# Kernel tuning notes

Measured on AMD Instinct MI355X. Metric: run time of the kernel, lower is better.

The kernel has to match this reference:

```python
import jax, jax.numpy as jnp
import numpy as np

HEADS = 8
EPS = 1e-5


def setup_inputs() -> dict:
    key = jax.random.key(0)
    ks = jax.random.split(key, 8)
    B, S, D = 4, 2048, 512
    inputs = jax.random.normal(ks[0], (B, S, D), dtype=jnp.float32)
    mask = jnp.ones((B, S), dtype=jnp.int32)
    sc = 1.0 / np.sqrt(D)
    # torch Linear weights stored transposed as [in, out] for x @ W
    W_qkv = jax.random.uniform(ks[1], (D, 3 * D), jnp.float32, -sc, sc)
    b_qkv = jax.random.uniform(ks[2], (3 * D,), jnp.float32, -sc, sc)
    W_o = jax.random.uniform(ks[3], (D, D), jnp.float32, -sc, sc)
    b_o = jax.random.uniform(ks[4], (D,), jnp.float32, -sc, sc)
    gamma = jnp.ones((D,), jnp.float32)
    beta = jnp.zeros((D,), jnp.float32)
    return {"inputs": inputs, "mask": mask, "W_qkv": W_qkv, "b_qkv": b_qkv,
            "W_o": W_o, "b_o": b_o, "gamma": gamma, "beta": beta}


def reference(inputs, mask, W_qkv, b_qkv, W_o, b_o, gamma, beta):
    B, S, D = inputs.shape
    H = HEADS
    dh = D // H
    t = inputs @ W_qkv + b_qkv                      # [B,S,3D]
    q, k, v = jnp.split(t, 3, axis=-1)
    # [B,S,D] -> [B,H,S,dh]
    q = q.reshape(B, S, H, dh).transpose(0, 2, 1, 3)
    k = k.reshape(B, S, H, dh).transpose(0, 2, 1, 3)
    v = v.reshape(B, S, H, dh).transpose(0, 2, 1, 3)
    # unscaled dot-product attention (is_scaled=False in the source)
    scores = jnp.einsum('bhqd,bhkd->bhqk', q, k)    # [B,H,S,S]
    key_mask = (mask > 0)[:, None, None, :]         # broadcast over heads & query rows
    scores = jnp.where(key_mask, scores, -jnp.inf)
    attn = jax.nn.softmax(scores, axis=-1)
    att = jnp.einsum('bhqk,bhkd->bhqd', attn, v)    # [B,H,S,dh]
    att = att.transpose(0, 2, 1, 3).reshape(B, S, D)
    out = att @ W_o + b_o
    x = out + att                                    # residual
    mu = jnp.mean(x, axis=-1, keepdims=True)
    var = jnp.mean(jnp.square(x - mu), axis=-1, keepdims=True)
    return (x - mu) / jnp.sqrt(var + EPS) * gamma + beta
```

## Files before the change

kernel.cpp:

```cpp
#include <hip/hip_runtime.h>
#include <cstdint>

#define S_LEN 2048
#define D_MODEL 512
#define H_NUM 8
#define DH 64
#define LOG2E 1.4426950408889634f

typedef __attribute__((ext_vector_type(8))) short bf16x8;
typedef __attribute__((ext_vector_type(8))) unsigned short u16x8;
typedef __attribute__((ext_vector_type(4))) float f32x4;

__device__ inline unsigned short f2bf(float x) {
    unsigned int u = __builtin_bit_cast(unsigned int, x);
    u += 0x7fffu + ((u >> 16) & 1u);
    return (unsigned short)(u >> 16);
}
__device__ inline float bf2f(unsigned short u) {
    return __builtin_bit_cast(float, (unsigned int)u << 16);
}
__device__ inline unsigned pack_bf2(float a, float b) {
    unsigned ua = __builtin_bit_cast(unsigned, a) + 0x8000u;
    unsigned ub = __builtin_bit_cast(unsigned, b) + 0x8000u;
    return __builtin_amdgcn_perm(ub, ua, 0x07060302);
}

__device__ inline void async_ld16(const unsigned short* g, unsigned short* l) {
    __builtin_amdgcn_global_load_lds(
        (const __attribute__((address_space(1))) unsigned int*)(const unsigned int*)g,
        (__attribute__((address_space(3))) unsigned int*)(unsigned int*)l,
        16, 0, 0);
}

__global__ __launch_bounds__(256) void prep(
    const float* __restrict__ X, const float* __restrict__ Wqkv,
    const float* __restrict__ Wo,
    unsigned short* __restrict__ Xb, unsigned short* __restrict__ WqkvT,
    unsigned short* __restrict__ WoT)
{
    __shared__ float tile[32][36];
    const int blk = blockIdx.x;
    const int tid = threadIdx.x;
    if (blk < 1024) {
        const int base = blk * 4096 + tid * 16;
        #pragma unroll
        for (int i = 0; i < 4; ++i) {
            float4 v = *(const float4*)(X + base + i * 4);
            ushort4 o;
            o.x = f2bf(v.x); o.y = f2bf(v.y); o.z = f2bf(v.z); o.w = f2bf(v.w);
            *(ushort4*)(Xb + base + i * 4) = o;
        }
        return;
    }
    const float* src; unsigned short* dst; int N, t;
    if (blk < 1792) { src = Wqkv; dst = WqkvT; N = 1536; t = blk - 1024; }
    else            { src = Wo;   dst = WoT;   N = 512;  t = blk - 1792; }
    const int tnx = N / 32;
    const int bx = t % tnx;
    const int by = t / tnx;
    const int row = tid >> 3;
    const int c4  = (tid & 7) * 4;
    *(float4*)&tile[row][c4] = *(const float4*)(src + (size_t)(by * 32 + row) * N + bx * 32 + c4);
    __syncthreads();
    ushort4 o;
    o.x = f2bf(tile[c4 + 0][row]);
    o.y = f2bf(tile[c4 + 1][row]);
    o.z = f2bf(tile[c4 + 2][row]);
    o.w = f2bf(tile[c4 + 3][row]);
    *(ushort4*)(dst + (size_t)(bx * 32 + row) * 512 + by * 32 + c4) = o;
}

__global__ __launch_bounds__(256) void qkv_mfma(
    const unsigned short* __restrict__ Xb, const unsigned short* __restrict__ WT,
    const float* __restrict__ bias,
    unsigned short* __restrict__ Q, unsigned short* __restrict__ K,
    unsigned short* __restrict__ Vt)
{
    __shared__ unsigned short sA[128 * 64];
    __shared__ unsigned short sB[128 * 64];
    const int tid  = threadIdx.x;
    const int w    = tid >> 6;
    const int lane = tid & 63;
    const int l16  = lane & 15;
    const int quad = lane >> 4;
    const int wm = w >> 1, wn = w & 1;
    const int n0 = blockIdx.x * 128;
    const int m0 = blockIdx.y * 128;

    const unsigned short* gA[4]; const unsigned short* gB[4];
    unsigned short *lA[4], *lB[4];
    #pragma unroll
    for (int j = 0; j < 4; ++j) {
        const int ci = tid + j * 256;
        const int row = ci >> 3;
        const int col = ((ci & 7) ^ (row & 7)) * 8;
        gA[j] = Xb + (size_t)(m0 + row) * 512 + col;
        gB[j] = WT + (size_t)(n0 + row) * 512 + col;
        lA[j] = sA + ci * 8 - lane * 8;
        lB[j] = sB + ci * 8 - lane * 8;
    }

    f32x4 acc[4][4] = {};
    for (int k0 = 0; k0 < 512; k0 += 64) {
        __syncthreads();
        #pragma unroll
        for (int j = 0; j < 4; ++j) {
            async_ld16(gA[j] + k0, lA[j]);
            async_ld16(gB[j] + k0, lB[j]);
        }
        __syncthreads();
        bf16x8 a[4][2], bfr[4][2];
        #pragma unroll
        for (int mi = 0; mi < 4; ++mi) {
            const int row = wm * 64 + mi * 16 + l16;
            a[mi][0] = *(const bf16x8*)&sA[row * 64 + ((quad       ^ (row & 7)) * 8)];
            a[mi][1] = *(const bf16x8*)&sA[row * 64 + (((4 + quad) ^ (row & 7)) * 8)];
        }
        #pragma unroll
        for (int ni = 0; ni < 4; ++ni) {
            const int row = wn * 64 + ni * 16 + l16;
            bfr[ni][0] = *(const bf16x8*)&sB[row * 64 + ((quad       ^ (row & 7)) * 8)];
            bfr[ni][1] = *(const bf16x8*)&sB[row * 64 + (((4 + quad) ^ (row & 7)) * 8)];
        }
        #pragma unroll
        for (int mi = 0; mi < 4; ++mi)
            #pragma unroll
            for (int ni = 0; ni < 4; ++ni) {
                acc[mi][ni] = __builtin_amdgcn_mfma_f32_16x16x32_bf16(a[mi][0], bfr[ni][0], acc[mi][ni], 0, 0, 0);
                acc[mi][ni] = __builtin_amdgcn_mfma_f32_16x16x32_bf16(a[mi][1], bfr[ni][1], acc[mi][ni], 0, 0, 0);
            }
    }

    const int which = n0 >> 9;
    const int h = ((n0 & 511) >> 6) + wn;
    const int b = m0 >> 11;
    const int sbase = (m0 & 2047) + wm * 64;
    float bv[4];
    #pragma unroll
    for (int ni = 0; ni < 4; ++ni) bv[ni] = bias[n0 + wn * 64 + ni * 16 + l16];
    if (which == 2) {
        #pragma unroll
        for (int ni = 0; ni < 4; ++ni) {
            const int dh = ni * 16 + l16;
            unsigned short* vp = Vt + ((size_t)(b * H_NUM + h) * DH + dh) * S_LEN;
            #pragma unroll
            for (int mi = 0; mi < 4; ++mi) {
                const int s0 = sbase + mi * 16 + quad * 4;
                ushort4 o;
                o.x = f2bf(acc[mi][ni][0] + bv[ni]);
                o.y = f2bf(acc[mi][ni][1] + bv[ni]);
                o.z = f2bf(acc[mi][ni][2] + bv[ni]);
                o.w = f2bf(acc[mi][ni][3] + bv[ni]);
                *(ushort4*)(vp + s0) = o;
            }
        }
    } else {
        const float qs = (which == 0) ? LOG2E : 1.0f;
        unsigned short* dst = (which == 0) ? Q : K;
        dst += (size_t)(b * H_NUM + h) * S_LEN * DH;
        #pragma unroll
        for (int mi = 0; mi < 4; ++mi)
            #pragma unroll
            for (int r = 0; r < 4; ++r) {
                const int s = sbase + mi * 16 + quad * 4 + r;
                #pragma unroll
                for (int ni = 0; ni < 4; ++ni)
                    dst[(size_t)s * DH + ni * 16 + l16] = f2bf((acc[mi][ni][r] + bv[ni]) * qs);
            }
    }
}

__global__ __launch_bounds__(256, 2) void attn_mfma(
    const unsigned short* __restrict__ Q, const unsigned short* __restrict__ K,
    const unsigned short* __restrict__ Vt, const int* __restrict__ mask,
    unsigned short* __restrict__ att)
{
    __shared__ __align__(16) char smem[38400];
    unsigned short* sK  = (unsigned short*)smem;
    unsigned short* sVt = (unsigned short*)(smem + 16384);
    unsigned short* sP  = (unsigned short*)(smem + 32768);
    float* smbt = (float*)(smem + 37888);
    float* red  = (float*)smem;
    float* lred = (float*)(smem + 34816);

    const int tid  = threadIdx.x;
    const int w    = tid >> 6;
    const int lane = tid & 63;
    const int l16  = lane & 15;
    const int quad = lane >> 4;
    const int qg = w >> 1;
    const int kg = w & 1;
    const int qt = blockIdx.x;
    const int bh = blockIdx.y;
    const int b  = bh >> 3;
    const int h  = bh & 7;
    const size_t kbase = (size_t)bh * S_LEN * DH;
    const size_t vbase = (size_t)bh * DH * S_LEN;
    unsigned short* sPw = sP + w * 640;

    bf16x8 qf[4][2];
    {
        const unsigned short* qp = Q + kbase + (size_t)(qt * 128 + qg * 64 + l16) * DH + quad * 8;
        #pragma unroll
        for (int t = 0; t < 4; ++t) {
            qf[t][0] = *(const bf16x8*)(qp + t * 16 * DH);
            qf[t][1] = *(const bf16x8*)(qp + t * 16 * DH + 32);
        }
    }

    const int ci0 = w * 128 + lane;
    const int ci1 = ci0 + 64;
    const int r0_ = ci0 >> 3, c0_ = ((ci0 & 7) ^ (r0_ & 7)) * 8;
    const int r1_ = ci1 >> 3, c1_ = ((ci1 & 7) ^ (r1_ & 7)) * 8;
    const int kOff0 = r0_ * 64 + c0_;
    const int kOff1 = r1_ * 64 + c1_;
    const int vOff0 = r0_ * S_LEN + c0_;
    const int vOff1 = r1_ * S_LEN + c1_;
    const int lds0 = ci0 * 8 - lane * 8;
    const int lds1 = ci1 * 8 - lane * 8;

    bf16x8 vones;
    #pragma unroll
    for (int j = 0; j < 8; ++j) vones[j] = (short)0x3F80;

    f32x4 O[4][4] = {};
    f32x4 Ol[4] = {};

    {
        const unsigned short* gK = K  + kbase;
        const unsigned short* gV = Vt + vbase;
        async_ld16(gK + kOff0, sK + lds0);
        async_ld16(gK + kOff1, sK + lds1);
        async_ld16(gV + vOff0, sVt + lds0);
        async_ld16(gV + vOff1, sVt + lds1);
        if (tid < 64) smbt[tid] = mask[b * S_LEN + tid] ? 0.f : -1e30f;
    }

    for (int kt = 0; kt < 32; ++kt) {
        const int cur = kt & 1, nxt = cur ^ 1;
        __syncthreads();
        if (kt + 1 < 32) {
            const unsigned short* gK = K  + kbase + (size_t)(kt + 1) * 64 * DH;
            const unsigned short* gV = Vt + vbase + (kt + 1) * 64;
            async_ld16(gK + kOff0, sK + nxt * 4096 + lds0);
            async_ld16(gK + kOff1, sK + nxt * 4096 + lds1);
            async_ld16(gV + vOff0, sVt + nxt * 4096 + lds0);
            async_ld16(gV + vOff1, sVt + nxt * 4096 + lds1);
            if (tid < 64) smbt[nxt * 64 + tid] = mask[b * S_LEN + (kt + 1) * 64 + tid] ? 0.f : -1e30f;
        }
        const unsigned short* sKc = sK  + cur * 4096;
        const unsigned short* sVc = sVt + cur * 4096;

        bf16x8 kb[2][2];
        #pragma unroll
        for (int kpb = 0; kpb < 2; ++kpb) {
            const int row = kg * 32 + kpb * 16 + l16;
            const int x = row & 7;
            kb[kpb][0] = *(const bf16x8*)&sKc[row * 64 + ((quad       ^ x) * 8)];
            kb[kpb][1] = *(const bf16x8*)&sKc[row * 64 + (((4 + quad) ^ x) * 8)];
        }
        float4 mb[2];
        #pragma unroll
        for (int kpb = 0; kpb < 2; ++kpb)
            mb[kpb] = *(const float4*)&smbt[cur * 64 + kg * 32 + kpb * 16 + quad * 4];

        bf16x8 vb[4];
        #pragma unroll
        for (int db = 0; db < 4; ++db) {
            const int row = db * 16 + l16;
            const int x = row & 7;
            vb[db] = *(const bf16x8*)&sVc[row * 64 + (((4 * kg + quad) ^ x) * 8)];
        }

        #pragma unroll
        for (int t = 0; t < 4; ++t) {
            f32x4 c0 = {0,0,0,0}, c1 = {0,0,0,0};
            c0 = __builtin_amdgcn_mfma_f32_16x16x32_bf16(kb[0][0], qf[t][0], c0, 0, 0, 0);
            c0 = __builtin_amdgcn_mfma_f32_16x16x32_bf16(kb[0][1], qf[t][1], c0, 0, 0, 0);
            c1 = __builtin_amdgcn_mfma_f32_16x16x32_bf16(kb[1][0], qf[t][0], c1, 0, 0, 0);
            c1 = __builtin_amdgcn_mfma_f32_16x16x32_bf16(kb[1][1], qf[t][1], c1, 0, 0, 0);

            const float p00 = __builtin_amdgcn_exp2f(c0[0] + mb[0].x);
            const float p01 = __builtin_amdgcn_exp2f(c0[1] + mb[0].y);
            const float p02 = __builtin_amdgcn_exp2f(c0[2] + mb[0].z);
            const float p03 = __builtin_amdgcn_exp2f(c0[3] + mb[0].w);
            const float p10 = __builtin_amdgcn_exp2f(c1[0] + mb[1].x);
            const float p11 = __builtin_amdgcn_exp2f(c1[1] + mb[1].y);
            const float p12 = __builtin_amdgcn_exp2f(c1[2] + mb[1].z);
            const float p13 = __builtin_amdgcn_exp2f(c1[3] + mb[1].w);
            uint2 pk0, pk1;
            pk0.x = pack_bf2(p00, p01); pk0.y = pack_bf2(p02, p03);
            pk1.x = pack_bf2(p10, p11); pk1.y = pack_bf2(p12, p13);
            *(uint2*)&sPw[l16 * 40 + quad * 4]      = pk0;
            *(uint2*)&sPw[l16 * 40 + 16 + quad * 4] = pk1;

            const bf16x8 pa = *(const bf16x8*)&sPw[l16 * 40 + quad * 8];
            #pragma unroll
            for (int db = 0; db < 4; ++db)
                O[t][db] = __builtin_amdgcn_mfma_f32_16x16x32_bf16(pa, vb[db], O[t][db], 0, 0, 0);
            Ol[t] = __builtin_amdgcn_mfma_f32_16x16x32_bf16(pa, vones, Ol[t], 0, 0, 0);
        }
    }

    __syncthreads();
    if (kg == 1) {
        #pragma unroll
        for (int t = 0; t < 4; ++t) {
            #pragma unroll
            for (int db = 0; db < 4; ++db) {
                #pragma unroll
                for (int r = 0; r < 4; ++r)
                    red[(size_t)(qg * 64 + t * 16 + quad * 4 + r) * 68 + db * 16 + l16] = O[t][db][r];
            }
            if (l16 == 0) {
                #pragma unroll
                for (int r = 0; r < 4; ++r)
                    lred[qg * 64 + t * 16 + quad * 4 + r] = Ol[t][r];
            }
        }
    }
    __syncthreads();
    if (kg == 0) {
        #pragma unroll
        for (int t = 0; t < 4; ++t) {
            #pragma unroll
            for (int r = 0; r < 4; ++r) {
                const int lrow = qg * 64 + t * 16 + quad * 4 + r;
                const float l = Ol[t][r] + lred[lrow];
                const float invr = 1.0f / l;
                const size_t grow = (size_t)b * S_LEN + qt * 128 + lrow;
                unsigned short* op = att + grow * D_MODEL + h * DH + l16;
                #pragma unroll
                for (int db = 0; db < 4; ++db) {
                    const float v = (O[t][db][r] + red[(size_t)lrow * 68 + db * 16 + l16]) * invr;
                    op[db * 16] = f2bf(v);
                }
            }
        }
    }
}

__global__ __launch_bounds__(256) void proj_mfma(
    const unsigned short* __restrict__ attb, const unsigned short* __restrict__ WoT,
    const float* __restrict__ bo, float* __restrict__ xbuf)
{
    __shared__ unsigned short sA[128 * 64];
    __shared__ unsigned short sB[64 * 64];
    const int tid  = threadIdx.x;
    const int w    = tid >> 6;
    const int lane = tid & 63;
    const int l16  = lane & 15;
    const int quad = lane >> 4;
    const int wm = w >> 1, wn = w & 1;
    const int n0 = blockIdx.x * 64;
    const int m0 = blockIdx.y * 128;

    const unsigned short* gA[4]; unsigned short* lA[4];
    const unsigned short* gB[2]; unsigned short* lB[2];
    #pragma unroll
    for (int j = 0; j < 4; ++j) {
        const int ci = tid + j * 256;
        const int row = ci >> 3;
        const int col = ((ci & 7) ^ (row & 7)) * 8;
        gA[j] = attb + (size_t)(m0 + row) * 512 + col;
        lA[j] = sA + ci * 8 - lane * 8;
    }
    #pragma unroll
    for (int j = 0; j < 2; ++j) {
        const int ci = tid + j * 256;
        const int row = ci >> 3;
        const int col = ((ci & 7) ^ (row & 7)) * 8;
        gB[j] = WoT + (size_t)(n0 + row) * 512 + col;
        lB[j] = sB + ci * 8 - lane * 8;
    }

    f32x4 acc[4][2] = {};
    for (int k0 = 0; k0 < 512; k0 += 64) {
        __syncthreads();
        #pragma unroll
        for (int j = 0; j < 4; ++j) async_ld16(gA[j] + k0, lA[j]);
        #pragma unroll
        for (int j = 0; j < 2; ++j) async_ld16(gB[j] + k0, lB[j]);
        __syncthreads();
        bf16x8 a[4][2], bfr[2][2];
        #pragma unroll
        for (int mi = 0; mi < 4; ++mi) {
            const int row = wm * 64 + mi * 16 + l16;
            a[mi][0] = *(const bf16x8*)&sA[row * 64 + ((quad       ^ (row & 7)) * 8)];
            a[mi][1] = *(const bf16x8*)&sA[row * 64 + (((4 + quad) ^ (row & 7)) * 8)];
        }
        #pragma unroll
        for (int ni = 0; ni < 2; ++ni) {
            const int row = wn * 32 + ni * 16 + l16;
            bfr[ni][0] = *(const bf16x8*)&sB[row * 64 + ((quad       ^ (row & 7)) * 8)];
            bfr[ni][1] = *(const bf16x8*)&sB[row * 64 + (((4 + quad) ^ (row & 7)) * 8)];
        }
        #pragma unroll
        for (int mi = 0; mi < 4; ++mi)
            #pragma unroll
            for (int ni = 0; ni < 2; ++ni) {
                acc[mi][ni] = __builtin_amdgcn_mfma_f32_16x16x32_bf16(a[mi][0], bfr[ni][0], acc[mi][ni], 0, 0, 0);
                acc[mi][ni] = __builtin_amdgcn_mfma_f32_16x16x32_bf16(a[mi][1], bfr[ni][1], acc[mi][ni], 0, 0, 0);
            }
    }

    #pragma unroll
    for (int ni = 0; ni < 2; ++ni) {
        const int n = n0 + wn * 32 + ni * 16 + l16;
        const float bv = bo[n];
        #pragma unroll
        for (int mi = 0; mi < 4; ++mi) {
            #pragma unroll
            for (int r = 0; r < 4; ++r) {
                const int m = m0 + wm * 64 + mi * 16 + quad * 4 + r;
                const float resid = bf2f(attb[(size_t)m * 512 + n]);
                xbuf[(size_t)m * 512 + n] = acc[mi][ni][r] + bv + resid;
            }
        }
    }
}

__global__ __launch_bounds__(256) void ln_kernel(
    const float* __restrict__ xbuf, const float* __restrict__ gamma,
    const float* __restrict__ beta, float* __restrict__ out)
{
    const int tid = threadIdx.x;
    const int w = tid >> 6, lane = tid & 63;
    const size_t row = (size_t)blockIdx.x * 4 + w;
    const float* xp = xbuf + row * 512 + lane * 8;
    float4 v0 = *(const float4*)xp;
    float4 v1 = *(const float4*)(xp + 4);
    float s  = v0.x + v0.y + v0.z + v0.w + v1.x + v1.y + v1.z + v1.w;
    float sq = v0.x*v0.x + v0.y*v0.y + v0.z*v0.z + v0.w*v0.w
             + v1.x*v1.x + v1.y*v1.y + v1.z*v1.z + v1.w*v1.w;
    #pragma unroll
    for (int off = 1; off < 64; off <<= 1) {
        s  += __shfl_xor(s, off, 64);
        sq += __shfl_xor(sq, off, 64);
    }
    const float mu = s * (1.0f / 512.0f);
    const float var = sq * (1.0f / 512.0f) - mu * mu;
    const float rs = rsqrtf(var + 1e-5f);
    float4 g0 = *(const float4*)(gamma + lane * 8);
    float4 g1 = *(const float4*)(gamma + lane * 8 + 4);
    float4 b0 = *(const float4*)(beta + lane * 8);
    float4 b1 = *(const float4*)(beta + lane * 8 + 4);
    float4 o0, o1;
    o0.x = (v0.x - mu) * rs * g0.x + b0.x;
    o0.y = (v0.y - mu) * rs * g0.y + b0.y;
    o0.z = (v0.z - mu) * rs * g0.z + b0.z;
    o0.w = (v0.w - mu) * rs * g0.w + b0.w;
    o1.x = (v1.x - mu) * rs * g1.x + b1.x;
    o1.y = (v1.y - mu) * rs * g1.y + b1.y;
    o1.z = (v1.z - mu) * rs * g1.z + b1.z;
    o1.w = (v1.w - mu) * rs * g1.w + b1.w;
    float* op = out + row * 512 + lane * 8;
    *(float4*)op = o0;
    *(float4*)(op + 4) = o1;
}

extern "C" void kernel_launch(void* const* d_in, const int* in_sizes, int n_in,
                              void* d_out, int out_size, void* d_ws, size_t ws_size,
                              hipStream_t stream)
{
    (void)in_sizes; (void)n_in; (void)out_size; (void)ws_size;
    const float* X    = (const float*)d_in[0];
    const int*   mask = (const int*)d_in[1];
    const float* Wqkv = (const float*)d_in[2];
    const float* bqkv = (const float*)d_in[3];
    const float* Wo   = (const float*)d_in[4];
    const float* bo   = (const float*)d_in[5];
    const float* gamma= (const float*)d_in[6];
    const float* beta = (const float*)d_in[7];
    float* out = (float*)d_out;

    const size_t NE = (size_t)4 * S_LEN * D_MODEL;
    unsigned short* ws16 = (unsigned short*)d_ws;
    unsigned short* Xb     = ws16;
    unsigned short* WqkvT  = Xb + NE;
    unsigned short* WoT    = WqkvT + 786432;
    unsigned short* Q      = WoT + 262144;
    unsigned short* K      = Q + NE;
    unsigned short* Vt     = K + NE;
    unsigned short* attb   = Vt + NE;
    float* xbuf = (float*)(attb + NE);

    prep<<<dim3(2048), 256, 0, stream>>>(X, Wqkv, Wo, Xb, WqkvT, WoT);
    qkv_mfma<<<dim3(12, 64), 256, 0, stream>>>(Xb, WqkvT, bqkv, Q, K, Vt);
    attn_mfma<<<dim3(16, 32), 256, 0, stream>>>(Q, K, Vt, mask, attb);
    proj_mfma<<<dim3(8, 64), 256, 0, stream>>>(attb, WoT, bo, xbuf);
    ln_kernel<<<dim3(2048), 256, 0, stream>>>(xbuf, gamma, beta, out);
}
```

Before: 180.9 us.

## Split attention over key halves, keep P in registers, add reduce kernel

Splits the key dimension of the attention kernel into two halves on a third grid axis, so twice as many blocks run, and adds a small reduce kernel that sums the two partial outputs and divides by the row sums. Key rows are permuted so the exp'd scores already sit in the MFMA A-operand layout, which removes the LDS round trip for P. The row sum is now built with VALU adds and shuffles instead of an extra MFMA against a ones vector. Occupancy is raised to 3 blocks per CU. In exchange the partial outputs are stored in bf16 to a workspace and read back, which adds traffic, a kernel launch and some rounding error. The unnormalised softmax without max subtraction is unchanged.

```diff
diff --git a/kernel.cpp b/kernel.cpp
--- a/kernel.cpp
+++ b/kernel.cpp
@@ -170,16 +170,15 @@
     }
 }
 
-__global__ __launch_bounds__(256, 2) void attn_mfma(
+__global__ __launch_bounds__(256, 3) void attn_mfma(
     const unsigned short* __restrict__ Q, const unsigned short* __restrict__ K,
     const unsigned short* __restrict__ Vt, const int* __restrict__ mask,
-    unsigned short* __restrict__ att)
-{
-    __shared__ __align__(16) char smem[38400];
+    unsigned short* __restrict__ Opart, float* __restrict__ lpart)
+{
+    __shared__ __align__(16) char smem[36864];
     unsigned short* sK  = (unsigned short*)smem;
     unsigned short* sVt = (unsigned short*)(smem + 16384);
-    unsigned short* sP  = (unsigned short*)(smem + 32768);
-    float* smbt = (float*)(smem + 37888);
+    float* smbt = (float*)(smem + 32768);
     float* red  = (float*)smem;
     float* lred = (float*)(smem + 34816);
 
@@ -192,11 +191,12 @@
     const int kg = w & 1;
     const int qt = blockIdx.x;
     const int bh = blockIdx.y;
+    const int z  = blockIdx.z;
     const int b  = bh >> 3;
     const int h  = bh & 7;
     const size_t kbase = (size_t)bh * S_LEN * DH;
     const size_t vbase = (size_t)bh * DH * S_LEN;
-    unsigned short* sPw = sP + w * 640;
+    const int kt0 = z * 16;
 
     bf16x8 qf[4][2];
     {
@@ -219,34 +219,32 @@
     const int lds0 = ci0 * 8 - lane * 8;
     const int lds1 = ci1 * 8 - lane * 8;
 
-    bf16x8 vones;
-    #pragma unroll
-    for (int j = 0; j < 8; ++j) vones[j] = (short)0x3F80;
-
     f32x4 O[4][4] = {};
-    f32x4 Ol[4] = {};
+    float lacc[4] = {};
+
+    const int prow = (l16 >> 2) * 8 + (l16 & 3);
 
     {
-        const unsigned short* gK = K  + kbase;
-        const unsigned short* gV = Vt + vbase;
+        const unsigned short* gK = K  + kbase + (size_t)kt0 * 64 * DH;
+        const unsigned short* gV = Vt + vbase + kt0 * 64;
         async_ld16(gK + kOff0, sK + lds0);
         async_ld16(gK + kOff1, sK + lds1);
         async_ld16(gV + vOff0, sVt + lds0);
         async_ld16(gV + vOff1, sVt + lds1);
-        if (tid < 64) smbt[tid] = mask[b * S_LEN + tid] ? 0.f : -1e30f;
-    }
-
-    for (int kt = 0; kt < 32; ++kt) {
+        if (tid < 64) smbt[tid] = mask[b * S_LEN + kt0 * 64 + tid] ? 0.f : -1e30f;
+    }
+
+    for (int kt = 0; kt < 16; ++kt) {
         const int cur = kt & 1, nxt = cur ^ 1;
         __syncthreads();
-        if (kt + 1 < 32) {
-            const unsigned short* gK = K  + kbase + (size_t)(kt + 1) * 64 * DH;
-            const unsigned short* gV = Vt + vbase + (kt + 1) * 64;
+        if (kt + 1 < 16) {
+            const unsigned short* gK = K  + kbase + (size_t)(kt0 + kt + 1) * 64 * DH;
+            const unsigned short* gV = Vt + vbase + (kt0 + kt + 1) * 64;
             async_ld16(gK + kOff0, sK + nxt * 4096 + lds0);
             async_ld16(gK + kOff1, sK + nxt * 4096 + lds1);
             async_ld16(gV + vOff0, sVt + nxt * 4096 + lds0);
             async_ld16(gV + vOff1, sVt + nxt * 4096 + lds1);
-            if (tid < 64) smbt[nxt * 64 + tid] = mask[b * S_LEN + (kt + 1) * 64 + tid] ? 0.f : -1e30f;
+            if (tid < 64) smbt[nxt * 64 + tid] = mask[b * S_LEN + (kt0 + kt + 1) * 64 + tid] ? 0.f : -1e30f;
         }
         const unsigned short* sKc = sK  + cur * 4096;
         const unsigned short* sVc = sVt + cur * 4096;
@@ -254,22 +252,20 @@
         bf16x8 kb[2][2];
         #pragma unroll
         for (int kpb = 0; kpb < 2; ++kpb) {
-            const int row = kg * 32 + kpb * 16 + l16;
+            const int row = kg * 32 + prow + kpb * 4;
             const int x = row & 7;
             kb[kpb][0] = *(const bf16x8*)&sKc[row * 64 + ((quad       ^ x) * 8)];
             kb[kpb][1] = *(const bf16x8*)&sKc[row * 64 + (((4 + quad) ^ x) * 8)];
         }
-        float4 mb[2];
-        #pragma unroll
-        for (int kpb = 0; kpb < 2; ++kpb)
-            mb[kpb] = *(const float4*)&smbt[cur * 64 + kg * 32 + kpb * 16 + quad * 4];
+        float4 mb0 = *(const float4*)&smbt[cur * 64 + kg * 32 + quad * 8];
+        float4 mb1 = *(const float4*)&smbt[cur * 64 + kg * 32 + quad * 8 + 4];
 
         bf16x8 vb[4];
         #pragma unroll
         for (int db = 0; db < 4; ++db) {
             const int row = db * 16 + l16;
             const int x = row & 7;
-            vb[db] = *(const bf16x8*)&sVc[row * 64 + (((4 * kg + quad) ^ x) * 8)];
+            vb[db] = *(const bf16x8*)&sVc[row * 64 + (((kg * 4 + quad) ^ x) * 8)];
         }
 
         #pragma unroll
@@ -280,64 +276,87 @@
             c1 = __builtin_amdgcn_mfma_f32_16x16x32_bf16(kb[1][0], qf[t][0], c1, 0, 0, 0);
             c1 = __builtin_amdgcn_mfma_f32_16x16x32_bf16(kb[1][1], qf[t][1], c1, 0, 0, 0);
 
-            const float p00 = __builtin_amdgcn_exp2f(c0[0] + mb[0].x);
-            const float p01 = __builtin_amdgcn_exp2f(c0[1] + mb[0].y);
-            const float p02 = __builtin_amdgcn_exp2f(c0[2] + mb[0].z);
-            const float p03 = __builtin_amdgcn_exp2f(c0[3] + mb[0].w);
-            const float p10 = __builtin_amdgcn_exp2f(c1[0] + mb[1].x);
-            const float p11 = __builtin_amdgcn_exp2f(c1[1] + mb[1].y);
-            const float p12 = __builtin_amdgcn_exp2f(c1[2] + mb[1].z);
-            const float p13 = __builtin_amdgcn_exp2f(c1[3] + mb[1].w);
-            uint2 pk0, pk1;
-            pk0.x = pack_bf2(p00, p01); pk0.y = pack_bf2(p02, p03);
-            pk1.x = pack_bf2(p10, p11); pk1.y = pack_bf2(p12, p13);
-            *(uint2*)&sPw[l16 * 40 + quad * 4]      = pk0;
-            *(uint2*)&sPw[l16 * 40 + 16 + quad * 4] = pk1;
-
-            const bf16x8 pa = *(const bf16x8*)&sPw[l16 * 40 + quad * 8];
+            const float p0 = __builtin_amdgcn_exp2f(c0[0] + mb0.x);
+            const float p1 = __builtin_amdgcn_exp2f(c0[1] + mb0.y);
+            const float p2 = __builtin_amdgcn_exp2f(c0[2] + mb0.z);
+            const float p3 = __builtin_amdgcn_exp2f(c0[3] + mb0.w);
+            const float p4 = __builtin_amdgcn_exp2f(c1[0] + mb1.x);
+            const float p5 = __builtin_amdgcn_exp2f(c1[1] + mb1.y);
+            const float p6 = __builtin_amdgcn_exp2f(c1[2] + mb1.z);
+            const float p7 = __builtin_amdgcn_exp2f(c1[3] + mb1.w);
+            lacc[t] += ((p0 + p1) + (p2 + p3)) + ((p4 + p5) + (p6 + p7));
+
+            uint4 paw;
+            paw.x = pack_bf2(p0, p1);
+            paw.y = pack_bf2(p2, p3);
+            paw.z = pack_bf2(p4, p5);
+            paw.w = pack_bf2(p6, p7);
+            const bf16x8 pa = __builtin_bit_cast(bf16x8, paw);
             #pragma unroll
             for (int db = 0; db < 4; ++db)
                 O[t][db] = __builtin_amdgcn_mfma_f32_16x16x32_bf16(pa, vb[db], O[t][db], 0, 0, 0);
-            Ol[t] = __builtin_amdgcn_mfma_f32_16x16x32_bf16(pa, vones, Ol[t], 0, 0, 0);
-        }
-    }
-
+        }
+    }
+
+    #pragma unroll
+    for (int t = 0; t < 4; ++t) {
+        lacc[t] += __shfl_xor(lacc[t], 16, 64);
+        lacc[t] += __shfl_xor(lacc[t], 32, 64);
+    }
     __syncthreads();
+    if (quad == 0) {
+        #pragma unroll
+        for (int t = 0; t < 4; ++t)
+            lred[kg * 128 + qg * 64 + t * 16 + l16] = lacc[t];
+    }
     if (kg == 1) {
         #pragma unroll
-        for (int t = 0; t < 4; ++t) {
-            #pragma unroll
-            for (int db = 0; db < 4; ++db) {
+        for (int t = 0; t < 4; ++t)
+            #pragma unroll
+            for (int db = 0; db < 4; ++db)
                 #pragma unroll
                 for (int r = 0; r < 4; ++r)
                     red[(size_t)(qg * 64 + t * 16 + quad * 4 + r) * 68 + db * 16 + l16] = O[t][db][r];
-            }
-            if (l16 == 0) {
-                #pragma unroll
-                for (int r = 0; r < 4; ++r)
-                    lred[qg * 64 + t * 16 + quad * 4 + r] = Ol[t][r];
-            }
-        }
     }
     __syncthreads();
     if (kg == 0) {
+        const size_t zoff = (size_t)z * 8192;
         #pragma unroll
         for (int t = 0; t < 4; ++t) {
             #pragma unroll
             for (int r = 0; r < 4; ++r) {
                 const int lrow = qg * 64 + t * 16 + quad * 4 + r;
-                const float l = Ol[t][r] + lred[lrow];
-                const float invr = 1.0f / l;
                 const size_t grow = (size_t)b * S_LEN + qt * 128 + lrow;
-                unsigned short* op = att + grow * D_MODEL + h * DH + l16;
-                #pragma unroll
-                for (int db = 0; db < 4; ++db) {
-                    const float v = (O[t][db][r] + red[(size_t)lrow * 68 + db * 16 + l16]) * invr;
-                    op[db * 16] = f2bf(v);
-                }
+                unsigned short* op = Opart + (zoff + grow) * 512 + h * DH + l16;
+                op[0]  = f2bf(O[t][0][r] + red[(size_t)lrow * 68 +  0 + l16]);
+                op[16] = f2bf(O[t][1][r] + red[(size_t)lrow * 68 + 16 + l16]);
+                op[32] = f2bf(O[t][2][r] + red[(size_t)lrow * 68 + 32 + l16]);
+                op[48] = f2bf(O[t][3][r] + red[(size_t)lrow * 68 + 48 + l16]);
+                if (l16 == 0)
+                    lpart[(zoff + grow) * 8 + h] = lred[lrow] + lred[128 + lrow];
             }
         }
     }
+}
+
+__global__ __launch_bounds__(256) void attn_reduce(
+    const unsigned short* __restrict__ Opart, const float* __restrict__ lpart,
+    unsigned short* __restrict__ attb)
+{
+    const int tid = threadIdx.x;
+    const int w = tid >> 6, lane = tid & 63;
+    const size_t row = (size_t)blockIdx.x * 4 + w;
+    const int c0 = lane * 8;
+    const int h = lane >> 3;
+    const float l = lpart[row * 8 + h] + lpart[(8192 + row) * 8 + h];
+    const float inv = 1.0f / l;
+    u16x8 a = *(const u16x8*)(Opart + row * 512 + c0);
+    u16x8 bq = *(const u16x8*)(Opart + (size_t)(8192 + row) * 512 + c0);
+    u16x8 o;
+    #pragma unroll
+    for (int j = 0; j < 8; ++j)
+        o[j] = f2bf((bf2f(a[j]) + bf2f(bq[j])) * inv);
+    *(u16x8*)(attb + row * 512 + c0) = o;
 }
 
 __global__ __launch_bounds__(256) void proj_mfma(
@@ -484,10 +503,13 @@
     unsigned short* Vt     = K + NE;
     unsigned short* attb   = Vt + NE;
     float* xbuf = (float*)(attb + NE);
+    unsigned short* Opart = (unsigned short*)xbuf;
+    float* lpart = xbuf + NE;
 
     prep<<<dim3(2048), 256, 0, stream>>>(X, Wqkv, Wo, Xb, WqkvT, WoT);
     qkv_mfma<<<dim3(12, 64), 256, 0, stream>>>(Xb, WqkvT, bqkv, Q, K, Vt);
-    attn_mfma<<<dim3(16, 32), 256, 0, stream>>>(Q, K, Vt, mask, attb);
+    attn_mfma<<<dim3(16, 32, 2), 256, 0, stream>>>(Q, K, Vt, mask, Opart, lpart);
+    attn_reduce<<<dim3(2048), 256, 0, stream>>>(Opart, lpart, attb);
     proj_mfma<<<dim3(8, 64), 256, 0, stream>>>(attb, WoT, bo, xbuf);
     ln_kernel<<<dim3(2048), 256, 0, stream>>>(xbuf, gamma, beta, out);
 }
```

After: 255.1 us. 1.41x slower.
